# Kernel tuning notes

Measured on AMD Instinct MI355X. Metric: run time of the kernel, lower is better.

The kernel has to match this reference:

```python
import jax, jax.numpy as jnp
import numpy as np

E, B, S, C, N, D, DFF, H, K_FREQ = 4, 16, 256, 17, 16, 32, 64, 4, 4
DH = D // H
MA_KERNELS = (4, 8, 12)


def setup_inputs() -> dict:
    key = jax.random.key(0)
    ks = jax.random.split(key, 16)
    sc = 1.0 / np.sqrt(D).astype(np.float32)
    inp = {
        "x": jax.random.normal(ks[0], (B, S, C, 1), jnp.float32),
        "original_x": jax.random.uniform(ks[1], (B, S, 2), jnp.float32),
        "start_W": jax.random.normal(ks[2], (D,), jnp.float32),
        "start_b": jnp.zeros((D,), jnp.float32),
        "Wq": jax.random.normal(ks[3], (E, D, D), jnp.float32) * sc,
        "Wk": jax.random.normal(ks[4], (E, D, D), jnp.float32) * sc,
        "Wv": jax.random.normal(ks[5], (E, D, D), jnp.float32) * sc,
        "Wo": jax.random.normal(ks[6], (E, D, D), jnp.float32) * sc,
        "ln1_g": jnp.ones((E, D), jnp.float32),
        "ln1_b": jnp.zeros((E, D), jnp.float32),
        "ln2_g": jnp.ones((E, D), jnp.float32),
        "ln2_b": jnp.zeros((E, D), jnp.float32),
        "W1": jax.random.normal(ks[7], (E, D, DFF), jnp.float32) * sc,
        "b1": jnp.zeros((E, DFF), jnp.float32),
        "W2": jax.random.normal(ks[8], (E, DFF, D), jnp.float32) * (1.0 / np.sqrt(DFF).astype(np.float32)),
        "b2": jnp.zeros((E, D), jnp.float32),
    }
    return inp


def _moving_avg(x, k):
    # x: [B,S,Ch], replicate-pad then uniform window of size k (stride 1)
    front = jnp.repeat(x[:, :1], (k - 1) // 2, axis=1)
    end = jnp.repeat(x[:, -1:], k // 2, axis=1)
    xp = jnp.concatenate([front, x, end], axis=1)  # [B, S+k-1, Ch]
    c = jnp.cumsum(xp, axis=1)
    c = jnp.concatenate([jnp.zeros_like(c[:, :1]), c], axis=1)
    return (c[:, k:] - c[:, :-k]) / jnp.asarray(k, x.dtype)


def _fourier_season(x, k):
    # ETSformer-style FourierLayer: keep top-k amplitude frequencies (excluding DC)
    s = x.shape[1]
    xf = jnp.fft.rfft(x, axis=1)            # [B,F,Ch] complex
    amp = jnp.abs(xf)
    amp = amp.at[:, 0, :].set(-jnp.inf)     # exclude DC
    topv = jax.lax.top_k(jnp.moveaxis(amp, 1, -1), k)[0]  # [B,Ch,k]
    thresh = topv[..., -1]                  # [B,Ch]
    mask = amp >= thresh[:, None, :]
    xf_m = jnp.where(mask, xf, 0)
    return jnp.fft.irfft(xf_m, n=s, axis=1).astype(x.dtype)


def _ln(z, g, b):
    m = jnp.mean(z, -1, keepdims=True)
    v = jnp.var(z, -1, keepdims=True)
    return (z - m) * jax.lax.rsqrt(v + 1e-5) * g + b


def _expert_fwd(args):
    h, wq, wk, wv, wo, g1, bg1, g2, bg2, w1, b1e, w2, b2e = args
    # h: [B,S,N,D]; pre-LN MHA over the sequence axis per (batch, node)
    z = _ln(h, g1, bg1)
    q = jnp.einsum('bsnd,de->bsne', z, wq).reshape(B, S, N, H, DH)
    k_ = jnp.einsum('bsnd,de->bsne', z, wk).reshape(B, S, N, H, DH)
    v_ = jnp.einsum('bsnd,de->bsne', z, wv).reshape(B, S, N, H, DH)
    att = jnp.einsum('bqnhd,bknhd->bnhqk', q, k_) * (1.0 / np.sqrt(DH).astype(np.float32))
    att = jax.nn.softmax(att, axis=-1)
    o = jnp.einsum('bnhqk,bknhd->bqnhd', att, v_).reshape(B, S, N, D)
    h = h + jnp.einsum('bsnd,de->bsne', o, wo)
    z2 = _ln(h, g2, bg2)
    f = jax.nn.relu(jnp.einsum('bsnd,df->bsnf', z2, w1) + b1e)
    h = h + jnp.einsum('bsnf,fd->bsnd', f, w2) + b2e
    return h


def reference(x, original_x, start_W, start_b, Wq, Wk, Wv, Wo,
              ln1_g, ln1_b, ln2_g, ln2_b, W1, b1, W2, b2):
    xc = x[:, :, :, 0]                                  # [B,S,C]
    trend = sum(_moving_avg(xc, k) for k in MA_KERNELS) / float(len(MA_KERNELS))
    season = _fourier_season(xc, K_FREQ)
    new_x = xc + season + trend                         # [B,S,C]

    scores = original_x[:, :, -1]                       # [B,S]
    bins = jnp.linspace(scores.min(), scores.max(), E + 1)
    assign = jnp.clip(jnp.searchsorted(bins, scores, side='right') - 1, 0, E - 1)  # [B,S] int

    xns = new_x[:, :, :-1]                              # [B,S,N] drop score channel
    onehot = (assign[None] == jnp.arange(E)[:, None, None])          # [E,B,S] bool
    expert_in = xns[None] * onehot[..., None].astype(xns.dtype)      # [E,B,S,N] dense zero-padded dispatch
    hidden = expert_in[..., None] * start_W + start_b                # [E,B,S,N,D] start_linear

    outs = jax.lax.map(_expert_fwd, (hidden, Wq, Wk, Wv, Wo,
                                     ln1_g, ln1_b, ln2_g, ln2_b, W1, b1, W2, b2))  # [E,B,S,N,D]
    combined = jnp.einsum('ebs,ebsnd->bsnd', onehot.astype(outs.dtype), outs)      # one-hot combine
    return combined
```

## Files before the change

kernel.cpp:

```cpp
#include <hip/hip_runtime.h>
#include <math.h>

#define BB 16
#define SS 256
#define CC 17
#define NCH 16
#define DD 32
#define DFFN 64
#define HH 4
#define DH 8
#define EE 4

#define WS_K0 16
#define WS_V0 144
#define WS_XNS 512
#define WS_SPI (WS_XNS + BB*SS*NCH)
#define WS_Q   (WS_SPI + BB*SS + 64)
#define WS_KVU (WS_Q + BB*SS*NCH*DD)
#define WS_WT  (WS_KVU + BB*SS*NCH*32)
#define WS_WL  (WS_WT + 6144)

#define PRE 0.51006977f

typedef __fp16 hv2 __attribute__((ext_vector_type(2)));

__device__ __forceinline__ unsigned pkh2(float a, float b) {
  hv2 r = __builtin_amdgcn_cvt_pkrtz(a, b);
  unsigned u; __builtin_memcpy(&u, &r, 4);
  return u;
}
__device__ __forceinline__ float fd2(unsigned a, unsigned b, float c) {
  hv2 av, bv;
  __builtin_memcpy(&av, &a, 4);
  __builtin_memcpy(&bv, &b, 4);
  return __builtin_amdgcn_fdot2(av, bv, c, false);
}
__device__ __forceinline__ float h2lo(unsigned u) {
  hv2 v; __builtin_memcpy(&v, &u, 4); return (float)v[0];
}
__device__ __forceinline__ float h2hi(unsigned u) {
  hv2 v; __builtin_memcpy(&v, &u, 4); return (float)v[1];
}

__global__ void decomp_prep_kernel(const float* __restrict__ x,
                                   const float* __restrict__ ox,
                                   const float* __restrict__ sb,
                                   const float* __restrict__ g1,
                                   const float* __restrict__ bb1,
                                   const float* __restrict__ Wq,
                                   const float* __restrict__ Wk,
                                   const float* __restrict__ Wv,
                                   const float* __restrict__ Wo,
                                   const float* __restrict__ W1,
                                   const float* __restrict__ W2,
                                   float* __restrict__ ws) {
  const int t = threadIdx.x;
  if (blockIdx.x < 256) {
    const int b = blockIdx.x / NCH;
    const int c = blockIdx.x % NCH;
    __shared__ float xs[SS];
    __shared__ float pr[256], pi[256];
    __shared__ float amp[129];
    __shared__ float2 YY[129];
    __shared__ float sth;
    xs[t] = x[(b*SS + t)*CC + c];
    __syncthreads();
    const float TH0 = 0.024543692606170259f;
    {
      const int f = (t & 127) + 1;
      const int half = t >> 7;
      float s1, c1; sincosf(TH0*(float)f, &s1, &c1);
      const int ph0 = (f * half * 128) & 255;
      float cr, si; sincosf(TH0*(float)ph0, &si, &cr);
      float xr = 0.f, xi = 0.f;
      for (int s2 = 0; s2 < 128; ++s2) {
        float xvv = xs[half*128 + s2];
        xr += xvv * cr;
        xi -= xvv * si;
        float nc = cr*c1 - si*s1;
        si = si*c1 + cr*s1;
        cr = nc;
      }
      pr[t] = xr; pi[t] = xi;
    }
    __syncthreads();
    if (t < 128) {
      float xr = pr[t] + pr[t+128];
      float xi = pi[t] + pi[t+128];
      pr[t] = xr; pi[t] = xi;
      amp[t+1] = sqrtf(xr*xr + xi*xi);
    }
    __syncthreads();
    if (t < 64) {
      float a0 = amp[t+1], a1 = amp[t+65];
      int i0 = t+1, i1 = t+65;
      float th = -1e30f;
      for (int r = 0; r < 4; ++r) {
        float mv = (a0 > a1) ? a0 : a1;
        int   mi = (a0 > a1) ? i0 : i1;
        for (int off = 32; off > 0; off >>= 1) {
          float ov = __shfl_xor(mv, off);
          int   oi = __shfl_xor(mi, off);
          if (ov > mv || (ov == mv && oi < mi)) { mv = ov; mi = oi; }
        }
        th = mv;
        if (mi == i0) a0 = -1e30f;
        if (mi == i1) a1 = -1e30f;
      }
      if (t == 0) sth = th;
    }
    __syncthreads();
    if (t < 128) {
      const int f = t + 1;
      float wgt = (amp[f] >= sth) ? ((f == 128) ? 1.0f : 2.0f) * (1.0f/256.0f) : 0.0f;
      YY[f] = make_float2(wgt * pr[t], wgt * pi[t]);
    }
    __syncthreads();
    float s1, c1; sincosf(TH0*(float)t, &s1, &c1);
    float cr = c1, si = s1, acc = 0.f;
    for (int f = 1; f <= 128; ++f) {
      float2 y = YY[f];
      acc += y.x*cr - y.y*si;
      float nc = cr*c1 - si*s1;
      si = si*c1 + cr*s1;
      cr = nc;
    }
    const float season = acc;
    float s4 = 0.f, s8 = 0.f, s12 = 0.f;
    #pragma unroll
    for (int j = 0; j < 4; ++j)  { int p = t + j - 1; p = p < 0 ? 0 : (p > SS-1 ? SS-1 : p); s4  += xs[p]; }
    #pragma unroll
    for (int j = 0; j < 8; ++j)  { int p = t + j - 3; p = p < 0 ? 0 : (p > SS-1 ? SS-1 : p); s8  += xs[p]; }
    #pragma unroll
    for (int j = 0; j < 12; ++j) { int p = t + j - 5; p = p < 0 ? 0 : (p > SS-1 ? SS-1 : p); s12 += xs[p]; }
    float trend = (s4 * 0.25f + s8 * 0.125f + s12 * (1.0f/12.0f)) * (1.0f/3.0f);
    ws[WS_XNS + (b*SS + t)*NCH + c] = xs[t] + season + trend;
  } else if (blockIdx.x < 272) {
    const int b = blockIdx.x - 256;
    __shared__ float red[8];
    __shared__ int asg[SS];
    __shared__ int cnt[EE];
    __shared__ float z0[EE*DD];
    float mn = 3e38f, mx = -3e38f;
    for (int i = t; i < BB*SS; i += 256) {
      float v = ox[2*i + 1];
      mn = fminf(mn, v); mx = fmaxf(mx, v);
    }
    for (int off = 32; off > 0; off >>= 1) {
      mn = fminf(mn, __shfl_xor(mn, off));
      mx = fmaxf(mx, __shfl_xor(mx, off));
    }
    if ((t & 63) == 0) { red[(t>>6)*2] = mn; red[(t>>6)*2+1] = mx; }
    __syncthreads();
    mn = fminf(fminf(red[0], red[2]), fminf(red[4], red[6]));
    mx = fmaxf(fmaxf(red[1], red[3]), fmaxf(red[5], red[7]));
    const float step = (mx - mn) * 0.25f;
    const float e1 = mn + step, e2 = mn + 2.f*step, e3 = mn + 3.f*step;
    float sc = ox[(b*SS + t)*2 + 1];
    asg[t] = (sc >= e1) + (sc >= e2) + (sc >= e3);
    __syncthreads();
    if (t < EE) {
      int c = 0;
      for (int s2 = 0; s2 < SS; ++s2) c += (asg[s2] == t);
      cnt[t] = c;
    }
    __syncthreads();
    int* SPw  = (int*)ws + WS_SPI;
    int* OFFw = SPw + BB*SS;
    if (t < EE) {
      int off = 0;
      for (int i = 0; i < t; ++i) off += cnt[i];
      OFFw[b*EE + t] = off;
      int kp = off;
      for (int s2 = 0; s2 < SS; ++s2) if (asg[s2] == t) SPw[b*SS + (kp++)] = s2;
    }
    if (t < 128) {
      int ee = t >> 5, d = t & 31;
      float m = 0.f;
      for (int i = 0; i < DD; ++i) m += sb[i];
      m *= (1.0f/DD);
      float var = 0.f;
      for (int i = 0; i < DD; ++i) { float df = sb[i]-m; var += df*df; }
      var *= (1.0f/DD);
      float rs = rsqrtf(var + 1e-5f);
      z0[ee*DD + d] = (sb[d]-m)*rs*g1[ee*DD+d] + bb1[ee*DD+d];
    }
    __syncthreads();
    if (b == 0 && t < 128) {
      int ee = t >> 5, d = t & 31;
      float k0 = 0.f, v0 = 0.f;
      for (int i = 0; i < DD; ++i) {
        float zz = z0[ee*DD + i];
        k0 += zz * Wk[ee*DD*DD + i*DD + d];
        v0 += zz * Wv[ee*DD*DD + i*DD + d];
      }
      ws[WS_K0 + ee*DD + d] = k0;
      ws[WS_V0 + ee*DD + d] = v0;
    }
  } else {
    unsigned* img = (unsigned*)ws + WS_WT;
    const int base_u = (blockIdx.x - 272)*1024;
    #pragma unroll
    for (int i = 0; i < 4; ++i) {
      int u = base_u + i*256 + t;
      unsigned val;
      if (u < 6144) {
        int mat = u >> 11, r = u & 2047;
        int row = r >> 4, ip = r & 15;
        int e = row >> 5, q = row & 31;
        int d = (q & 3)*8 + (q >> 2);
        const float* Wm = (mat == 0) ? Wq : (mat == 1) ? Wk : Wv;
        const float* src = Wm + e*1024 + d;
        val = pkh2(src[ip*64], src[ip*64 + 32]);
      } else {
        int v = u - 6144;
        if (v < 2048) {
          int row = v >> 4, ip = v & 15;
          int e = row >> 5, q = row & 31;
          int d = (q & 3)*8 + (q >> 2);
          const float* src = Wo + e*1024 + d;
          val = pkh2(src[ip*64], src[ip*64 + 32]);
        } else if (v < 6144) {
          int r = v - 2048;
          int row = r >> 4, ip = r & 15;
          int e = row >> 6, q = row & 63;
          int j = (q & 3)*16 + (q >> 2);
          const float* src = W1 + e*2048 + j;
          val = pkh2(src[ip*128], src[ip*128 + 64]);
        } else {
          int r = v - 6144;
          int a = r >> 11, rr = r & 2047;
          int row = rr >> 4, ip = rr & 15;
          int e = row >> 5, q = row & 31;
          int d = (q & 3)*8 + (q >> 2);
          int jp = a*16 + ip;
          const float* src = W2 + e*2048 + d;
          val = pkh2(src[2*jp*32], src[(2*jp+1)*32]);
        }
      }
      img[u] = val;
    }
  }
}

__launch_bounds__(256, 4)
__global__ void qkv_kernel(float* __restrict__ ws,
    const float* __restrict__ g1, const float* __restrict__ bb1,
    const float* __restrict__ sW, const float* __restrict__ sb) {
  __shared__ unsigned wT[6144];
  const int t = threadIdx.x;
  {
    const uint4* simg = (const uint4*)((const unsigned*)ws + WS_WT);
    uint4* dst = (uint4*)wT;
    #pragma unroll
    for (int i = 0; i < 6; ++i) dst[i*256 + t] = simg[i*256 + t];
  }
  const int gI = blockIdx.x*256 + t;
  const int hh = gI & 3;
  const int pos = gI >> 2;
  const int n = pos & 15;
  const int p = (pos >> 4) & 255;
  const int b = pos >> 12;
  const int* SP  = (const int*)ws + WS_SPI;
  const int* OFF = SP + BB*SS;
  const int o1 = OFF[b*4+1], o2 = OFF[b*4+2], o3 = OFF[b*4+3];
  const int e = (p >= o1) + (p >= o2) + (p >= o3);
  const int s = SP[b*SS + p];
  const float xv = ws[WS_XNS + (b*SS + s)*NCH + n];

  float h[DD];
  #pragma unroll
  for (int d = 0; d < DD; ++d) h[d] = xv * sW[d] + sb[d];
  float m = 0.f;
  #pragma unroll
  for (int d = 0; d < DD; ++d) m += h[d];
  m *= (1.0f/DD);
  float var = 0.f;
  #pragma unroll
  for (int d = 0; d < DD; ++d) { float df = h[d]-m; var += df*df; }
  var *= (1.0f/DD);
  float rs = rsqrtf(var + 1e-5f);
  unsigned zp[16];
  #pragma unroll
  for (int ip = 0; ip < 16; ++ip) {
    float za = (h[2*ip]  -m)*rs*g1[e*DD+2*ip]   + bb1[e*DD+2*ip];
    float zb = (h[2*ip+1]-m)*rs*g1[e*DD+2*ip+1] + bb1[e*DD+2*ip+1];
    zp[ip] = pkh2(za, zb);
  }
  __syncthreads();

  float q[DH], kk[DH], vv[DH];
  #pragma unroll
  for (int dd = 0; dd < DH; ++dd) {
    const int row16 = (e*32 + dd*4 + hh)*16;
    const uint4* rq = (const uint4*)&wT[row16];
    const uint4* rk = (const uint4*)&wT[2048 + row16];
    const uint4* rv = (const uint4*)&wT[4096 + row16];
    float aq = 0.f, ak = 0.f, av = 0.f;
    #pragma unroll
    for (int g4 = 0; g4 < 4; ++g4) {
      uint4 wq4 = rq[g4], wk4 = rk[g4], wv4 = rv[g4];
      aq = fd2(zp[4*g4+0], wq4.x, aq); aq = fd2(zp[4*g4+1], wq4.y, aq);
      aq = fd2(zp[4*g4+2], wq4.z, aq); aq = fd2(zp[4*g4+3], wq4.w, aq);
      ak = fd2(zp[4*g4+0], wk4.x, ak); ak = fd2(zp[4*g4+1], wk4.y, ak);
      ak = fd2(zp[4*g4+2], wk4.z, ak); ak = fd2(zp[4*g4+3], wk4.w, ak);
      av = fd2(zp[4*g4+0], wv4.x, av); av = fd2(zp[4*g4+1], wv4.y, av);
      av = fd2(zp[4*g4+2], wv4.z, av); av = fd2(zp[4*g4+3], wv4.w, av);
    }
    q[dd] = aq; kk[dd] = ak; vv[dd] = av;
  }
  float* qp = ws + WS_Q + pos*32 + hh*DH;
  ((float4*)qp)[0] = make_float4(q[0]*PRE, q[1]*PRE, q[2]*PRE, q[3]*PRE);
  ((float4*)qp)[1] = make_float4(q[4]*PRE, q[5]*PRE, q[6]*PRE, q[7]*PRE);
  unsigned* kvg = (unsigned*)ws + WS_KVU + ((b*NCH + n)*SS + p)*32 + hh*8;
  ((uint4*)kvg)[0] = make_uint4(pkh2(kk[0],kk[1]), pkh2(kk[2],kk[3]), pkh2(kk[4],kk[5]), pkh2(kk[6],kk[7]));
  ((uint4*)kvg)[1] = make_uint4(pkh2(vv[0],vv[1]), pkh2(vv[2],vv[3]), pkh2(vv[4],vv[5]), pkh2(vv[6],vv[7]));
}

__launch_bounds__(512, 4)
__global__ void attn_ffn_kernel(const float* __restrict__ ws,
    const float* __restrict__ sW, const float* __restrict__ sb,
    const float* __restrict__ g2, const float* __restrict__ bb2,
    const float* __restrict__ b1, const float* __restrict__ b2,
    float* __restrict__ out) {
  const int blk = blockIdx.x;
  const int hq = blk & 1;
  const int n = (blk >> 1) & 15;
  const int b = blk >> 5;
  const int t = threadIdx.x;
  const int wj = t >> 6;
  const int lane = t & 63;
  const int pg = lane >> 2;
  const int hh = lane & 3;
  const int g = hq + 2*wj;
  const int p = g*16 + pg;
  const int pb = wj*16 + pg;
  __shared__ unsigned lds[8192];
  __shared__ unsigned wl[10240];
  float* fl = (float*)lds;

  {
    const uint4* src = (const uint4*)((const unsigned*)ws + WS_KVU + (b*NCH + n)*8192);
    uint4* dst = (uint4*)lds;
    #pragma unroll
    for (int i = 0; i < 4; ++i) dst[i*512 + t] = src[i*512 + t];
  }
  {
    const uint4* src = (const uint4*)((const unsigned*)ws + WS_WL);
    uint4* dst = (uint4*)wl;
    #pragma unroll
    for (int i = 0; i < 5; ++i) dst[i*512 + t] = src[i*512 + t];
  }

  const int* SP  = (const int*)ws + WS_SPI;
  const int* OFF = SP + BB*SS;
  const int o1 = OFF[b*4+1], o2 = OFF[b*4+2], o3 = OFF[b*4+3];
  const int e = (p >= o1) + (p >= o2) + (p >= o3);
  const int beg = (e==0) ? 0  : ((e==1) ? o1 : ((e==2) ? o2 : o3));
  const int end = (e==0) ? o1 : ((e==1) ? o2 : ((e==2) ? o3 : SS));
  const int s = SP[b*SS + p];

  float qf[DH];
  {
    const float* qp = ws + WS_Q + ((b*SS + p)*NCH + n)*32 + hh*DH;
    float4 qa = ((const float4*)qp)[0];
    float4 qb = ((const float4*)qp)[1];
    qf[0]=qa.x; qf[1]=qa.y; qf[2]=qa.z; qf[3]=qa.w;
    qf[4]=qb.x; qf[5]=qb.y; qf[6]=qb.z; qf[7]=qb.w;
  }
  unsigned qp2[4];
  #pragma unroll
  for (int i = 0; i < 4; ++i) qp2[i] = pkh2(qf[2*i], qf[2*i+1]);
  float s0 = 0.f;
  #pragma unroll
  for (int d = 0; d < DH; ++d) s0 += qf[d] * ws[WS_K0 + e*DD + hh*DH + d];
  float v0s[DH];
  #pragma unroll
  for (int d = 0; d < DH; ++d) v0s[d] = ws[WS_V0 + e*DD + hh*DH + d];
  __syncthreads();

  float wsum = 0.f;
  float o[DH] = {0,0,0,0,0,0,0,0};
  for (int jk = beg; jk < end; ++jk) {
    uint4 ku = *(const uint4*)&lds[jk*32 + hh*8];
    uint4 vu = *(const uint4*)&lds[jk*32 + hh*8 + 4];
    float a = 0.f;
    a = fd2(qp2[0], ku.x, a); a = fd2(qp2[1], ku.y, a);
    a = fd2(qp2[2], ku.z, a); a = fd2(qp2[3], ku.w, a);
    float w = __builtin_amdgcn_exp2f(a);
    wsum += w;
    o[0] += w*h2lo(vu.x); o[1] += w*h2hi(vu.x);
    o[2] += w*h2lo(vu.y); o[3] += w*h2hi(vu.y);
    o[4] += w*h2lo(vu.z); o[5] += w*h2hi(vu.z);
    o[6] += w*h2lo(vu.w); o[7] += w*h2hi(vu.w);
  }
  const int nmis = SS - (end - beg);
  float w0 = (float)nmis * __builtin_amdgcn_exp2f(s0);
  wsum += w0;
  #pragma unroll
  for (int d = 0; d < DH; ++d) o[d] += w0 * v0s[d];
  float inv = 1.0f / wsum;
  #pragma unroll
  for (int d = 0; d < DH; ++d) o[d] *= inv;
  __syncthreads();

  #pragma unroll
  for (int d = 0; d < DH; ++d) fl[pb*33 + hh*DH + d] = o[d];
  __syncthreads();
  unsigned ovp[16];
  #pragma unroll
  for (int ip = 0; ip < 16; ++ip) ovp[ip] = pkh2(fl[pb*33 + 2*ip], fl[pb*33 + 2*ip+1]);

  const float xv = ws[WS_XNS + (b*SS + s)*NCH + n];
  float acc[DH];
  #pragma unroll
  for (int dd = 0; dd < DH; ++dd) {
    int d = hh*DH + dd;
    const uint4* row = (const uint4*)&wl[(e*32 + dd*4 + hh)*16];
    float a = xv * sW[d] + sb[d];
    #pragma unroll
    for (int g4 = 0; g4 < 4; ++g4) {
      uint4 w4 = row[g4];
      a = fd2(ovp[4*g4+0], w4.x, a); a = fd2(ovp[4*g4+1], w4.y, a);
      a = fd2(ovp[4*g4+2], w4.z, a); a = fd2(ovp[4*g4+3], w4.w, a);
    }
    acc[dd] = a;
  }
  __syncthreads();
  #pragma unroll
  for (int dd = 0; dd < DH; ++dd) fl[pb*33 + hh*DH + dd] = acc[dd];
  __syncthreads();

  float h2r[DD];
  #pragma unroll
  for (int i = 0; i < DD; ++i) h2r[i] = fl[pb*33 + i];
  float m = 0.f;
  #pragma unroll
  for (int d = 0; d < DD; ++d) m += h2r[d];
  m *= (1.0f/DD);
  float var = 0.f;
  #pragma unroll
  for (int d = 0; d < DD; ++d) { float df = h2r[d]-m; var += df*df; }
  var *= (1.0f/DD);
  float rs = rsqrtf(var + 1e-5f);
  unsigned zp2[16];
  #pragma unroll
  for (int ip = 0; ip < 16; ++ip) {
    float za = (h2r[2*ip]  -m)*rs*g2[e*DD+2*ip]   + bb2[e*DD+2*ip];
    float zb = (h2r[2*ip+1]-m)*rs*g2[e*DD+2*ip+1] + bb2[e*DD+2*ip+1];
    zp2[ip] = pkh2(za, zb);
  }
  float hres[DH];
  #pragma unroll
  for (int dd = 0; dd < DH; ++dd) hres[dd] = h2r[hh*DH + dd];
  __syncthreads();

  float f[16];
  #pragma unroll
  for (int jj = 0; jj < 16; ++jj) {
    const uint4* row = (const uint4*)&wl[2048 + (e*64 + jj*4 + hh)*16];
    float a = b1[e*DFFN + hh*16 + jj];
    #pragma unroll
    for (int g4 = 0; g4 < 4; ++g4) {
      uint4 w4 = row[g4];
      a = fd2(zp2[4*g4+0], w4.x, a); a = fd2(zp2[4*g4+1], w4.y, a);
      a = fd2(zp2[4*g4+2], w4.z, a); a = fd2(zp2[4*g4+3], w4.w, a);
    }
    f[jj] = fmaxf(a, 0.0f);
  }
  {
    uint4 fa = make_uint4(pkh2(f[0],f[1]), pkh2(f[2],f[3]), pkh2(f[4],f[5]), pkh2(f[6],f[7]));
    uint4 fb = make_uint4(pkh2(f[8],f[9]), pkh2(f[10],f[11]), pkh2(f[12],f[13]), pkh2(f[14],f[15]));
    *(uint4*)&lds[pb*36 + hh*8]     = fa;
    *(uint4*)&lds[pb*36 + hh*8 + 4] = fb;
  }
  __syncthreads();

  uint4 fpr[8];
  #pragma unroll
  for (int g4 = 0; g4 < 8; ++g4) fpr[g4] = *(const uint4*)&lds[pb*36 + 4*g4];
  float acc2[DH];
  #pragma unroll
  for (int dd = 0; dd < DH; ++dd) {
    int d = hh*DH + dd;
    const int row16 = (e*32 + dd*4 + hh)*16;
    float a = hres[dd] + b2[e*DD + d];
    #pragma unroll
    for (int g4 = 0; g4 < 8; ++g4) {
      const int plane = (g4 >> 2);
      uint4 w4 = *(const uint4*)&wl[6144 + plane*2048 + row16 + 4*(g4 & 3)];
      uint4 fq = fpr[g4];
      a = fd2(fq.x, w4.x, a); a = fd2(fq.y, w4.y, a);
      a = fd2(fq.z, w4.z, a); a = fd2(fq.w, w4.w, a);
    }
    acc2[dd] = a;
  }
  float* op = out + ((size_t)((b*SS + s)*NCH + n))*DD + hh*DH;
  *(float4*)(op)     = make_float4(acc2[0], acc2[1], acc2[2], acc2[3]);
  *(float4*)(op + 4) = make_float4(acc2[4], acc2[5], acc2[6], acc2[7]);
}

extern "C" void kernel_launch(void* const* d_in, const int* in_sizes, int n_in,
                              void* d_out, int out_size, void* d_ws, size_t ws_size,
                              hipStream_t stream) {
  (void)in_sizes; (void)n_in; (void)out_size; (void)ws_size;
  const float* x   = (const float*)d_in[0];
  const float* ox  = (const float*)d_in[1];
  const float* sW  = (const float*)d_in[2];
  const float* sb  = (const float*)d_in[3];
  const float* Wq  = (const float*)d_in[4];
  const float* Wk  = (const float*)d_in[5];
  const float* Wv  = (const float*)d_in[6];
  const float* Wo  = (const float*)d_in[7];
  const float* g1  = (const float*)d_in[8];
  const float* b1n = (const float*)d_in[9];
  const float* g2  = (const float*)d_in[10];
  const float* b2n = (const float*)d_in[11];
  const float* W1  = (const float*)d_in[12];
  const float* bf1 = (const float*)d_in[13];
  const float* W2  = (const float*)d_in[14];
  const float* bf2 = (const float*)d_in[15];
  float* out = (float*)d_out;
  float* ws  = (float*)d_ws;

  decomp_prep_kernel<<<288, 256, 0, stream>>>(x, ox, sb, g1, b1n,
                                              Wq, Wk, Wv, Wo, W1, W2, ws);
  qkv_kernel<<<BB*SS*NCH*4/256, 256, 0, stream>>>(ws, g1, b1n, sW, sb);
  attn_ffn_kernel<<<BB*NCH*2, 512, 0, stream>>>(ws, sW, sb, g2, b2n,
                                                bf1, bf2, out);
}
```

Before: 155.6 us.

## Fuse QKV projection into attention/FFN kernel and widen decomposition blocks

Merges the QKV kernel into the attention+FFN kernel, so each 1024-thread block handles one (batch, channel) pair. K/V are now written straight into LDS as fp16 and Q stays in registers, which removes the global round-trip through the Q and KV workspace buffers and one kernel launch. The prep kernel also moves to 1024 threads: the DFT and inverse DFT are split into more partial chunks and then reduced, which gives more parallelism per block. The costs are fewer blocks for the attention stage (256 instead of 512), 1024-thread blocks with a large LDS footprint that limit occupancy, and more register pressure.

```diff
diff --git a/kernel.cpp b/kernel.cpp
--- a/kernel.cpp
+++ b/kernel.cpp
@@ -15,9 +15,7 @@
 #define WS_V0 144
 #define WS_XNS 512
 #define WS_SPI (WS_XNS + BB*SS*NCH)
-#define WS_Q   (WS_SPI + BB*SS + 64)
-#define WS_KVU (WS_Q + BB*SS*NCH*DD)
-#define WS_WT  (WS_KVU + BB*SS*NCH*32)
+#define WS_WT  (WS_SPI + BB*SS + 64)
 #define WS_WL  (WS_WT + 6144)
 
 #define PRE 0.51006977f
@@ -42,6 +40,7 @@
   hv2 v; __builtin_memcpy(&v, &u, 4); return (float)v[1];
 }
 
+__launch_bounds__(1024)
 __global__ void decomp_prep_kernel(const float* __restrict__ x,
                                    const float* __restrict__ ox,
                                    const float* __restrict__ sb,
@@ -59,35 +58,38 @@
     const int b = blockIdx.x / NCH;
     const int c = blockIdx.x % NCH;
     __shared__ float xs[SS];
-    __shared__ float pr[256], pi[256];
+    __shared__ float prr[1024], pii[1024];
     __shared__ float amp[129];
     __shared__ float2 YY[129];
     __shared__ float sth;
-    xs[t] = x[(b*SS + t)*CC + c];
+    if (t < SS) xs[t] = x[(b*SS + t)*CC + c];
     __syncthreads();
     const float TH0 = 0.024543692606170259f;
     {
       const int f = (t & 127) + 1;
-      const int half = t >> 7;
+      const int chunk = t >> 7;
+      const int s0 = chunk * 32;
+      const int ph0 = (f * s0) & 255;
+      float si, cr; sincosf(TH0*(float)ph0, &si, &cr);
       float s1, c1; sincosf(TH0*(float)f, &s1, &c1);
-      const int ph0 = (f * half * 128) & 255;
-      float cr, si; sincosf(TH0*(float)ph0, &si, &cr);
       float xr = 0.f, xi = 0.f;
-      for (int s2 = 0; s2 < 128; ++s2) {
-        float xvv = xs[half*128 + s2];
+      #pragma unroll 4
+      for (int k = 0; k < 32; ++k) {
+        float xvv = xs[s0 + k];
         xr += xvv * cr;
         xi -= xvv * si;
         float nc = cr*c1 - si*s1;
         si = si*c1 + cr*s1;
         cr = nc;
       }
-      pr[t] = xr; pi[t] = xi;
+      prr[t] = xr; pii[t] = xi;
     }
     __syncthreads();
     if (t < 128) {
-      float xr = pr[t] + pr[t+128];
-      float xi = pi[t] + pi[t+128];
-      pr[t] = xr; pi[t] = xi;
+      float xr = 0.f, xi = 0.f;
+      #pragma unroll
+      for (int k2 = 0; k2 < 8; ++k2) { xr += prr[t + 128*k2]; xi += pii[t + 128*k2]; }
+      prr[t] = xr; pii[t] = xi;
       amp[t+1] = sqrtf(xr*xr + xi*xi);
     }
     __syncthreads();
@@ -113,37 +115,50 @@
     if (t < 128) {
       const int f = t + 1;
       float wgt = (amp[f] >= sth) ? ((f == 128) ? 1.0f : 2.0f) * (1.0f/256.0f) : 0.0f;
-      YY[f] = make_float2(wgt * pr[t], wgt * pi[t]);
-    }
-    __syncthreads();
-    float s1, c1; sincosf(TH0*(float)t, &s1, &c1);
-    float cr = c1, si = s1, acc = 0.f;
-    for (int f = 1; f <= 128; ++f) {
-      float2 y = YY[f];
-      acc += y.x*cr - y.y*si;
-      float nc = cr*c1 - si*s1;
-      si = si*c1 + cr*s1;
-      cr = nc;
-    }
-    const float season = acc;
-    float s4 = 0.f, s8 = 0.f, s12 = 0.f;
-    #pragma unroll
-    for (int j = 0; j < 4; ++j)  { int p = t + j - 1; p = p < 0 ? 0 : (p > SS-1 ? SS-1 : p); s4  += xs[p]; }
-    #pragma unroll
-    for (int j = 0; j < 8; ++j)  { int p = t + j - 3; p = p < 0 ? 0 : (p > SS-1 ? SS-1 : p); s8  += xs[p]; }
-    #pragma unroll
-    for (int j = 0; j < 12; ++j) { int p = t + j - 5; p = p < 0 ? 0 : (p > SS-1 ? SS-1 : p); s12 += xs[p]; }
-    float trend = (s4 * 0.25f + s8 * 0.125f + s12 * (1.0f/12.0f)) * (1.0f/3.0f);
-    ws[WS_XNS + (b*SS + t)*NCH + c] = xs[t] + season + trend;
+      YY[f] = make_float2(wgt * prr[t], wgt * pii[t]);
+    }
+    __syncthreads();
+    {
+      const int s = t & 255;
+      const int fc = t >> 8;
+      const int f0 = 1 + fc*32;
+      const int ph0 = (s * f0) & 255;
+      float si, cr; sincosf(TH0*(float)ph0, &si, &cr);
+      float s1, c1; sincosf(TH0*(float)s, &s1, &c1);
+      float acc = 0.f;
+      #pragma unroll 4
+      for (int k = 0; k < 32; ++k) {
+        float2 y = YY[f0 + k];
+        acc += y.x*cr - y.y*si;
+        float nc = cr*c1 - si*s1;
+        si = si*c1 + cr*s1;
+        cr = nc;
+      }
+      prr[t] = acc;
+    }
+    __syncthreads();
+    if (t < 256) {
+      float season = prr[t] + prr[t+256] + prr[t+512] + prr[t+768];
+      float s4 = 0.f, s8 = 0.f, s12 = 0.f;
+      #pragma unroll
+      for (int j = 0; j < 4; ++j)  { int p = t + j - 1; p = p < 0 ? 0 : (p > SS-1 ? SS-1 : p); s4  += xs[p]; }
+      #pragma unroll
+      for (int j = 0; j < 8; ++j)  { int p = t + j - 3; p = p < 0 ? 0 : (p > SS-1 ? SS-1 : p); s8  += xs[p]; }
+      #pragma unroll
+      for (int j = 0; j < 12; ++j) { int p = t + j - 5; p = p < 0 ? 0 : (p > SS-1 ? SS-1 : p); s12 += xs[p]; }
+      float trend = (s4 * 0.25f + s8 * 0.125f + s12 * (1.0f/12.0f)) * (1.0f/3.0f);
+      ws[WS_XNS + (b*SS + t)*NCH + c] = xs[t] + season + trend;
+    }
   } else if (blockIdx.x < 272) {
     const int b = blockIdx.x - 256;
-    __shared__ float red[8];
+    __shared__ float red[32];
     __shared__ int asg[SS];
     __shared__ int cnt[EE];
     __shared__ float z0[EE*DD];
     float mn = 3e38f, mx = -3e38f;
-    for (int i = t; i < BB*SS; i += 256) {
-      float v = ox[2*i + 1];
+    #pragma unroll
+    for (int k = 0; k < 4; ++k) {
+      float v = ox[(t + k*1024)*2 + 1];
       mn = fminf(mn, v); mx = fmaxf(mx, v);
     }
     for (int off = 32; off > 0; off >>= 1) {
@@ -152,12 +167,15 @@
     }
     if ((t & 63) == 0) { red[(t>>6)*2] = mn; red[(t>>6)*2+1] = mx; }
     __syncthreads();
-    mn = fminf(fminf(red[0], red[2]), fminf(red[4], red[6]));
-    mx = fmaxf(fmaxf(red[1], red[3]), fmaxf(red[5], red[7]));
+    mn = red[0]; mx = red[1];
+    #pragma unroll
+    for (int w = 1; w < 16; ++w) { mn = fminf(mn, red[w*2]); mx = fmaxf(mx, red[w*2+1]); }
     const float step = (mx - mn) * 0.25f;
     const float e1 = mn + step, e2 = mn + 2.f*step, e3 = mn + 3.f*step;
-    float sc = ox[(b*SS + t)*2 + 1];
-    asg[t] = (sc >= e1) + (sc >= e2) + (sc >= e3);
+    if (t < 256) {
+      float sc = ox[(b*SS + t)*2 + 1];
+      asg[t] = (sc >= e1) + (sc >= e2) + (sc >= e3);
+    }
     __syncthreads();
     if (t < EE) {
       int c = 0;
@@ -199,10 +217,10 @@
     }
   } else {
     unsigned* img = (unsigned*)ws + WS_WT;
-    const int base_u = (blockIdx.x - 272)*1024;
+    const int base_u = (blockIdx.x - 272)*4096;
     #pragma unroll
     for (int i = 0; i < 4; ++i) {
-      int u = base_u + i*256 + t;
+      int u = base_u + i*1024 + t;
       unsigned val;
       if (u < 6144) {
         int mat = u >> 11, r = u & 2047;
@@ -243,28 +261,37 @@
   }
 }
 
-__launch_bounds__(256, 4)
-__global__ void qkv_kernel(float* __restrict__ ws,
+__launch_bounds__(1024, 4)
+__global__ void fused_kernel(const float* __restrict__ ws,
     const float* __restrict__ g1, const float* __restrict__ bb1,
-    const float* __restrict__ sW, const float* __restrict__ sb) {
-  __shared__ unsigned wT[6144];
+    const float* __restrict__ sW, const float* __restrict__ sb,
+    const float* __restrict__ g2, const float* __restrict__ bb2,
+    const float* __restrict__ b1, const float* __restrict__ b2,
+    float* __restrict__ out) {
+  const int blk = blockIdx.x;
+  const int n = blk & 15;
+  const int b = blk >> 4;
   const int t = threadIdx.x;
+  const int p = t >> 2;
+  const int hh = t & 3;
+  __shared__ unsigned lds[24576];
+  float* fl = (float*)lds;
+  unsigned* wT = lds + 8192;
+  unsigned* wl = lds + 14336;
+
   {
     const uint4* simg = (const uint4*)((const unsigned*)ws + WS_WT);
     uint4* dst = (uint4*)wT;
     #pragma unroll
-    for (int i = 0; i < 6; ++i) dst[i*256 + t] = simg[i*256 + t];
-  }
-  const int gI = blockIdx.x*256 + t;
-  const int hh = gI & 3;
-  const int pos = gI >> 2;
-  const int n = pos & 15;
-  const int p = (pos >> 4) & 255;
-  const int b = pos >> 12;
+    for (int i = 0; i < 4; ++i) dst[i*1024 + t] = simg[i*1024 + t];
+  }
+
   const int* SP  = (const int*)ws + WS_SPI;
   const int* OFF = SP + BB*SS;
   const int o1 = OFF[b*4+1], o2 = OFF[b*4+2], o3 = OFF[b*4+3];
   const int e = (p >= o1) + (p >= o2) + (p >= o3);
+  const int beg = (e==0) ? 0  : ((e==1) ? o1 : ((e==2) ? o2 : o3));
+  const int end = (e==0) ? o1 : ((e==1) ? o2 : ((e==2) ? o3 : SS));
   const int s = SP[b*SS + p];
   const float xv = ws[WS_XNS + (b*SS + s)*NCH + n];
 
@@ -307,73 +334,18 @@
       av = fd2(zp[4*g4+0], wv4.x, av); av = fd2(zp[4*g4+1], wv4.y, av);
       av = fd2(zp[4*g4+2], wv4.z, av); av = fd2(zp[4*g4+3], wv4.w, av);
     }
-    q[dd] = aq; kk[dd] = ak; vv[dd] = av;
-  }
-  float* qp = ws + WS_Q + pos*32 + hh*DH;
-  ((float4*)qp)[0] = make_float4(q[0]*PRE, q[1]*PRE, q[2]*PRE, q[3]*PRE);
-  ((float4*)qp)[1] = make_float4(q[4]*PRE, q[5]*PRE, q[6]*PRE, q[7]*PRE);
-  unsigned* kvg = (unsigned*)ws + WS_KVU + ((b*NCH + n)*SS + p)*32 + hh*8;
-  ((uint4*)kvg)[0] = make_uint4(pkh2(kk[0],kk[1]), pkh2(kk[2],kk[3]), pkh2(kk[4],kk[5]), pkh2(kk[6],kk[7]));
-  ((uint4*)kvg)[1] = make_uint4(pkh2(vv[0],vv[1]), pkh2(vv[2],vv[3]), pkh2(vv[4],vv[5]), pkh2(vv[6],vv[7]));
-}
-
-__launch_bounds__(512, 4)
-__global__ void attn_ffn_kernel(const float* __restrict__ ws,
-    const float* __restrict__ sW, const float* __restrict__ sb,
-    const float* __restrict__ g2, const float* __restrict__ bb2,
-    const float* __restrict__ b1, const float* __restrict__ b2,
-    float* __restrict__ out) {
-  const int blk = blockIdx.x;
-  const int hq = blk & 1;
-  const int n = (blk >> 1) & 15;
-  const int b = blk >> 5;
-  const int t = threadIdx.x;
-  const int wj = t >> 6;
-  const int lane = t & 63;
-  const int pg = lane >> 2;
-  const int hh = lane & 3;
-  const int g = hq + 2*wj;
-  const int p = g*16 + pg;
-  const int pb = wj*16 + pg;
-  __shared__ unsigned lds[8192];
-  __shared__ unsigned wl[10240];
-  float* fl = (float*)lds;
-
-  {
-    const uint4* src = (const uint4*)((const unsigned*)ws + WS_KVU + (b*NCH + n)*8192);
-    uint4* dst = (uint4*)lds;
-    #pragma unroll
-    for (int i = 0; i < 4; ++i) dst[i*512 + t] = src[i*512 + t];
-  }
-  {
-    const uint4* src = (const uint4*)((const unsigned*)ws + WS_WL);
-    uint4* dst = (uint4*)wl;
-    #pragma unroll
-    for (int i = 0; i < 5; ++i) dst[i*512 + t] = src[i*512 + t];
-  }
-
-  const int* SP  = (const int*)ws + WS_SPI;
-  const int* OFF = SP + BB*SS;
-  const int o1 = OFF[b*4+1], o2 = OFF[b*4+2], o3 = OFF[b*4+3];
-  const int e = (p >= o1) + (p >= o2) + (p >= o3);
-  const int beg = (e==0) ? 0  : ((e==1) ? o1 : ((e==2) ? o2 : o3));
-  const int end = (e==0) ? o1 : ((e==1) ? o2 : ((e==2) ? o3 : SS));
-  const int s = SP[b*SS + p];
-
-  float qf[DH];
-  {
-    const float* qp = ws + WS_Q + ((b*SS + p)*NCH + n)*32 + hh*DH;
-    float4 qa = ((const float4*)qp)[0];
-    float4 qb = ((const float4*)qp)[1];
-    qf[0]=qa.x; qf[1]=qa.y; qf[2]=qa.z; qf[3]=qa.w;
-    qf[4]=qb.x; qf[5]=qb.y; qf[6]=qb.z; qf[7]=qb.w;
-  }
+    q[dd] = aq * PRE; kk[dd] = ak; vv[dd] = av;
+  }
+  *(uint4*)&lds[p*32 + hh*8]     = make_uint4(pkh2(kk[0],kk[1]), pkh2(kk[2],kk[3]),
+                                              pkh2(kk[4],kk[5]), pkh2(kk[6],kk[7]));
+  *(uint4*)&lds[p*32 + hh*8 + 4] = make_uint4(pkh2(vv[0],vv[1]), pkh2(vv[2],vv[3]),
+                                              pkh2(vv[4],vv[5]), pkh2(vv[6],vv[7]));
   unsigned qp2[4];
   #pragma unroll
-  for (int i = 0; i < 4; ++i) qp2[i] = pkh2(qf[2*i], qf[2*i+1]);
+  for (int i = 0; i < 4; ++i) qp2[i] = pkh2(q[2*i], q[2*i+1]);
   float s0 = 0.f;
   #pragma unroll
-  for (int d = 0; d < DH; ++d) s0 += qf[d] * ws[WS_K0 + e*DD + hh*DH + d];
+  for (int d = 0; d < DH; ++d) s0 += q[d] * ws[WS_K0 + e*DD + hh*DH + d];
   float v0s[DH];
   #pragma unroll
   for (int d = 0; d < DH; ++d) v0s[d] = ws[WS_V0 + e*DD + hh*DH + d];
@@ -405,13 +377,12 @@
   __syncthreads();
 
   #pragma unroll
-  for (int d = 0; d < DH; ++d) fl[pb*33 + hh*DH + d] = o[d];
+  for (int d = 0; d < DH; ++d) fl[p*33 + hh*DH + d] = o[d];
   __syncthreads();
   unsigned ovp[16];
   #pragma unroll
-  for (int ip = 0; ip < 16; ++ip) ovp[ip] = pkh2(fl[pb*33 + 2*ip], fl[pb*33 + 2*ip+1]);
-
-  const float xv = ws[WS_XNS + (b*SS + s)*NCH + n];
+  for (int ip = 0; ip < 16; ++ip) ovp[ip] = pkh2(fl[p*33 + 2*ip], fl[p*33 + 2*ip+1]);
+
   float acc[DH];
   #pragma unroll
   for (int dd = 0; dd < DH; ++dd) {
@@ -428,21 +399,21 @@
   }
   __syncthreads();
   #pragma unroll
-  for (int dd = 0; dd < DH; ++dd) fl[pb*33 + hh*DH + dd] = acc[dd];
+  for (int dd = 0; dd < DH; ++dd) fl[p*33 + hh*DH + dd] = acc[dd];
   __syncthreads();
 
   float h2r[DD];
   #pragma unroll
-  for (int i = 0; i < DD; ++i) h2r[i] = fl[pb*33 + i];
-  float m = 0.f;
+  for (int i = 0; i < DD; ++i) h2r[i] = fl[p*33 + i];
+  m = 0.f;
   #pragma unroll
   for (int d = 0; d < DD; ++d) m += h2r[d];
   m *= (1.0f/DD);
-  float var = 0.f;
+  var = 0.f;
   #pragma unroll
   for (int d = 0; d < DD; ++d) { float df = h2r[d]-m; var += df*df; }
   var *= (1.0f/DD);
-  float rs = rsqrtf(var + 1e-5f);
+  rs = rsqrtf(var + 1e-5f);
   unsigned zp2[16];
   #pragma unroll
   for (int ip = 0; ip < 16; ++ip) {
@@ -471,14 +442,14 @@
   {
     uint4 fa = make_uint4(pkh2(f[0],f[1]), pkh2(f[2],f[3]), pkh2(f[4],f[5]), pkh2(f[6],f[7]));
     uint4 fb = make_uint4(pkh2(f[8],f[9]), pkh2(f[10],f[11]), pkh2(f[12],f[13]), pkh2(f[14],f[15]));
-    *(uint4*)&lds[pb*36 + hh*8]     = fa;
-    *(uint4*)&lds[pb*36 + hh*8 + 4] = fb;
+    *(uint4*)&lds[p*36 + hh*8]     = fa;
+    *(uint4*)&lds[p*36 + hh*8 + 4] = fb;
   }
   __syncthreads();
 
   uint4 fpr[8];
   #pragma unroll
-  for (int g4 = 0; g4 < 8; ++g4) fpr[g4] = *(const uint4*)&lds[pb*36 + 4*g4];
+  for (int g4 = 0; g4 < 8; ++g4) fpr[g4] = *(const uint4*)&lds[p*36 + 4*g4];
   float acc2[DH];
   #pragma unroll
   for (int dd = 0; dd < DH; ++dd) {
@@ -523,9 +494,8 @@
   float* out = (float*)d_out;
   float* ws  = (float*)d_ws;
 
-  decomp_prep_kernel<<<288, 256, 0, stream>>>(x, ox, sb, g1, b1n,
-                                              Wq, Wk, Wv, Wo, W1, W2, ws);
-  qkv_kernel<<<BB*SS*NCH*4/256, 256, 0, stream>>>(ws, g1, b1n, sW, sb);
-  attn_ffn_kernel<<<BB*NCH*2, 512, 0, stream>>>(ws, sW, sb, g2, b2n,
-                                                bf1, bf2, out);
-}
+  decomp_prep_kernel<<<276, 1024, 0, stream>>>(x, ox, sb, g1, b1n,
+                                               Wq, Wk, Wv, Wo, W1, W2, ws);
+  fused_kernel<<<BB*NCH, 1024, 0, stream>>>(ws, g1, b1n, sW, sb, g2, b2n,
+                                            bf1, bf2, out);
+}
```

After: 145.6 us. 1.07x faster.
